# Kernel optimization log

Hardware: AMD Instinct MI355X
Metric: run time of the kernel (lower is better)

Reference implementation:

```python
import jax, jax.numpy as jnp
import numpy as np

N_EXPERTS = 8
TOP_K = 2
D_MODEL = 1024
HIDDEN = 4096


def setup_inputs() -> dict:
    key = jax.random.key(0)
    ks = jax.random.split(key, 6)
    B, S = 4, 1024
    scale = 0.02
    x = jax.random.normal(ks[0], (B, S, D_MODEL), dtype=jnp.float32)
    # gate / noise linear weights, torch nn.Linear convention: (out, in)
    w_gate = jax.random.normal(ks[1], (N_EXPERTS, D_MODEL), dtype=jnp.float32) * scale
    w_noise = jax.random.normal(ks[2], (N_EXPERTS, D_MODEL), dtype=jnp.float32) * scale
    # stacked expert weights: w_g/w_u: (E, H, D), w_d: (E, D, H)
    w_g = jax.random.normal(ks[3], (N_EXPERTS, HIDDEN, D_MODEL), dtype=jnp.float32) * scale
    w_u = jax.random.normal(ks[4], (N_EXPERTS, HIDDEN, D_MODEL), dtype=jnp.float32) * scale
    w_d = jax.random.normal(ks[5], (N_EXPERTS, D_MODEL, HIDDEN), dtype=jnp.float32) * scale
    return {"x": x, "w_gate": w_gate, "w_noise": w_noise, "w_g": w_g, "w_u": w_u, "w_d": w_d}


def reference(x, w_gate, w_noise, w_g, w_u, w_d):
    B, S, D = x.shape
    T = B * S
    xf = x.reshape(T, D)

    # --- NoisyTopKGate (eval mode: no noise) ---
    logits = xf @ w_gate.T                                  # (T, E)
    top_logits, top_idx = jax.lax.top_k(logits, TOP_K)      # (T, K)
    top_gates = jax.nn.softmax(top_logits, axis=-1)         # (T, K)
    rows = jnp.arange(T)[:, None]
    gates = jnp.zeros_like(logits).at[rows, top_idx].set(top_gates)  # (T, E) sparse

    probs = jax.nn.softmax(logits, axis=-1)
    f = gates.mean(axis=0)
    P = probs.mean(axis=0)
    aux_loss = N_EXPERTS * jnp.sum(f * P)

    # --- expert loop (SwiGLU FFN); gate==0 zeroes non-routed contributions ---
    out = jnp.zeros_like(xf)
    for e in range(N_EXPERTS):
        hidden = jax.nn.silu(xf @ w_g[e].T) * (xf @ w_u[e].T)   # (T, H)
        y = hidden @ w_d[e].T                                    # (T, D)
        out = out + gates[:, e:e + 1] * y

    return out.reshape(B, S, D), aux_loss
```

## Files before the change

### kernel.cpp

```cpp
#include <hip/hip_runtime.h>

#define TT 4096
#define DM 1024
#define HH 4096
#define NE 8
#define NSLOT (TT*2)
#define TM 128
#define MAXTILES 72

typedef __bf16 bf16x8 __attribute__((ext_vector_type(8)));
typedef float f32x4 __attribute__((ext_vector_type(4)));

__device__ __forceinline__ unsigned short f2bs(float f) {
  unsigned u = __float_as_uint(f);
  u += 0x7fffu + ((u >> 16) & 1u);
  return (unsigned short)(u >> 16);
}
__device__ __forceinline__ float bs2f(unsigned short s) {
  return __uint_as_float(((unsigned)s) << 16);
}
__device__ __forceinline__ unsigned pk_rnd(float lo, float hi) {
  return ((__float_as_uint(lo) + 0x8000u) >> 16) |
         ((__float_as_uint(hi) + 0x8000u) & 0xffff0000u);
}
__device__ __forceinline__ void gld_lds16(const unsigned short* g, unsigned short* l) {
  __builtin_amdgcn_global_load_lds(
      (const __attribute__((address_space(1))) unsigned int*)g,
      (__attribute__((address_space(3))) unsigned int*)l, 16, 0, 0);
}

__global__ __launch_bounds__(256) void k_gate(
    const float* __restrict__ x, const float* __restrict__ w_gate,
    int* __restrict__ counts, float* __restrict__ gsum, float* __restrict__ psum,
    int* __restrict__ gidx, float* __restrict__ gval) {
  __shared__ float wg[NE * DM];
  __shared__ float bg[NE]; __shared__ float bp[NE]; __shared__ int bc[NE];
  int tid = threadIdx.x;
  for (int i = tid; i < NE * DM; i += 256) wg[i] = w_gate[i];
  if (tid < NE) { bg[tid] = 0.f; bp[tid] = 0.f; bc[tid] = 0; }
  __syncthreads();
  int wave = tid >> 6, lane = tid & 63;
  for (int it = 0; it < 4; ++it) {
    int t = blockIdx.x * 16 + wave * 4 + it;
    const float* xr = x + (size_t)t * DM;
    float s[NE];
#pragma unroll
    for (int e = 0; e < NE; ++e) s[e] = 0.f;
    for (int d = lane; d < DM; d += 64) {
      float xv = xr[d];
#pragma unroll
      for (int e = 0; e < NE; ++e) s[e] += xv * wg[e * DM + d];
    }
#pragma unroll
    for (int e = 0; e < NE; ++e) {
      float v = s[e];
      v += __shfl_down(v, 32); v += __shfl_down(v, 16); v += __shfl_down(v, 8);
      v += __shfl_down(v, 4);  v += __shfl_down(v, 2);  v += __shfl_down(v, 1);
      s[e] = v;
    }
    if (lane == 0) {
      int e1 = 0; float v1 = s[0];
      for (int e = 1; e < NE; ++e) if (s[e] > v1) { v1 = s[e]; e1 = e; }
      int e2 = -1; float v2 = -1e30f;
      for (int e = 0; e < NE; ++e) if (e != e1 && s[e] > v2) { v2 = s[e]; e2 = e; }
      float g1 = 1.f / (1.f + __expf(v2 - v1));
      float g2 = 1.f - g1;
      float psm = 0.f, p[NE];
      for (int e = 0; e < NE; ++e) { p[e] = __expf(s[e] - v1); psm += p[e]; }
      float inv = 1.f / psm;
      atomicAdd(&bg[e1], g1); atomicAdd(&bg[e2], g2);
      for (int e = 0; e < NE; ++e) atomicAdd(&bp[e], p[e] * inv);
      atomicAdd(&bc[e1], 1); atomicAdd(&bc[e2], 1);
      gidx[t * 2] = e1; gidx[t * 2 + 1] = e2;
      gval[t * 2] = g1; gval[t * 2 + 1] = g2;
    }
  }
  __syncthreads();
  if (tid < NE) {
    atomicAdd(&counts[tid], bc[tid]);
    atomicAdd(&gsum[tid], bg[tid]);
    atomicAdd(&psum[tid], bp[tid]);
  }
}

__global__ void k_plan(const int* __restrict__ counts, const float* __restrict__ gsum,
                       const float* __restrict__ psum, int* __restrict__ bases,
                       int* __restrict__ ntiles, int* __restrict__ tile_e,
                       int* __restrict__ tile_s0, int* __restrict__ tile_n,
                       float* __restrict__ aux_out) {
  if (threadIdx.x != 0 || blockIdx.x != 0) return;
  int base = 0, nt = 0;
  for (int e = 0; e < NE; ++e) {
    bases[e] = base;
    int c = counts[e];
    for (int s = 0; s < c; s += TM) {
      tile_e[nt] = e; tile_s0[nt] = base + s;
      tile_n[nt] = (c - s < TM) ? (c - s) : TM; ++nt;
    }
    base += c;
  }
  *ntiles = nt;
  float aux = 0.f;
  for (int e = 0; e < NE; ++e)
    aux += (gsum[e] / (float)TT) * (psum[e] / (float)TT);
  *aux_out = aux * (float)NE;
}

__global__ __launch_bounds__(256) void k_scatter(
    const int* __restrict__ gidx, const int* __restrict__ bases,
    int* __restrict__ cursor, int* __restrict__ stok, int* __restrict__ t2s) {
  int t = blockIdx.x * 256 + threadIdx.x;
#pragma unroll
  for (int k = 0; k < 2; ++k) {
    int e = gidx[t * 2 + k];
    int pos = atomicAdd(&cursor[e], 1);
    int slot = bases[e] + pos;
    stok[slot] = t;
    t2s[t * 2 + k] = slot;
  }
}

__global__ __launch_bounds__(256) void k_gather(
    const float* __restrict__ x, const int* __restrict__ stok,
    unsigned short* __restrict__ abuf) {
  int gid = blockIdx.x * 256 + threadIdx.x;
  int slot = gid >> 7;
  int d0 = (gid & 127) << 3;
  int tok = stok[slot];
  const float* src = x + (size_t)tok * DM + d0;
  float4 v0 = *(const float4*)src;
  float4 v1 = *(const float4*)(src + 4);
  uint4 pk;
  pk.x = pk_rnd(v0.x, v0.y); pk.y = pk_rnd(v0.z, v0.w);
  pk.z = pk_rnd(v1.x, v1.y); pk.w = pk_rnd(v1.z, v1.w);
  *(uint4*)(abuf + (size_t)slot * DM + d0) = pk;
}


__global__ __launch_bounds__(256) void k_ffn1(
    const unsigned short* __restrict__ abuf, const float* __restrict__ w_g,
    const float* __restrict__ w_u, const int* __restrict__ ntiles,
    const int* __restrict__ tile_e, const int* __restrict__ tile_s0,
    const int* __restrict__ tile_n, unsigned short* __restrict__ hbuf) {
  int bid = blockIdx.x;
  int s = (bid & 7) * 576 + (bid >> 3);
  int mt = s % MAXTILES;
  int ny = s / MAXTILES;
  if (mt >= *ntiles) return;
  int e = tile_e[mt], s0 = tile_s0[mt], nrows = tile_n[mt];
  int n0 = ny * 64;
  __shared__ unsigned short As[TM * 64];
  __shared__ unsigned short Bg[64 * 64];
  __shared__ unsigned short Bu[64 * 64];
  int tid = threadIdx.x, wid = tid >> 6, lane = tid & 63;
  int wm = (wid >> 1) * 64, wn = (wid & 1) * 32;
  int l15 = lane & 15, lq = lane >> 4;
  int l8 = lane & 7, lr = lane >> 3;
  int scol = ((l8 ^ lr) << 3);

  const unsigned short* apA = abuf + (size_t)(s0 + wid * 32 + lr) * DM + scol;

  int br = tid >> 3, bb = tid & 7;
  int wb = ((bb ^ (br & 7)) << 3);
  const float* gp = w_g + ((size_t)e * HH + (size_t)(n0 + br)) * DM + bb * 8;
  const float* up = w_u + ((size_t)e * HH + (size_t)(n0 + br)) * DM + bb * 8;
  unsigned short* bg0 = Bg + br * 64 + wb;
  unsigned short* bu0 = Bu + br * 64 + wb;

  f32x4 accg[4][2], accu[4][2];
#pragma unroll
  for (int i = 0; i < 4; ++i)
#pragma unroll
    for (int j = 0; j < 2; ++j) {
      accg[i][j] = (f32x4){0.f, 0.f, 0.f, 0.f};
      accu[i][j] = (f32x4){0.f, 0.f, 0.f, 0.f};
    }

  for (int kb = 0; kb < DM; kb += 64) {
    __syncthreads();
#pragma unroll
    for (int c = 0; c < 4; ++c)
      gld_lds16(apA + kb + (size_t)c * 8 * DM, As + (wid * 32 + c * 8) * 64);
    float4 g0 = *(const float4*)(gp + kb);
    float4 g1 = *(const float4*)(gp + kb + 4);
    float4 g2 = *(const float4*)(gp + kb + (size_t)32 * DM);
    float4 g3 = *(const float4*)(gp + kb + (size_t)32 * DM + 4);
    float4 u0 = *(const float4*)(up + kb);
    float4 u1 = *(const float4*)(up + kb + 4);
    float4 u2 = *(const float4*)(up + kb + (size_t)32 * DM);
    float4 u3 = *(const float4*)(up + kb + (size_t)32 * DM + 4);
    uint4 p0, p1, q0, q1;
    p0.x = pk_rnd(g0.x, g0.y); p0.y = pk_rnd(g0.z, g0.w);
    p0.z = pk_rnd(g1.x, g1.y); p0.w = pk_rnd(g1.z, g1.w);
    p1.x = pk_rnd(g2.x, g2.y); p1.y = pk_rnd(g2.z, g2.w);
    p1.z = pk_rnd(g3.x, g3.y); p1.w = pk_rnd(g3.z, g3.w);
    q0.x = pk_rnd(u0.x, u0.y); q0.y = pk_rnd(u0.z, u0.w);
    q0.z = pk_rnd(u1.x, u1.y); q0.w = pk_rnd(u1.z, u1.w);
    q1.x = pk_rnd(u2.x, u2.y); q1.y = pk_rnd(u2.z, u2.w);
    q1.z = pk_rnd(u3.x, u3.y); q1.w = pk_rnd(u3.z, u3.w);
    *(uint4*)bg0 = p0;
    *(uint4*)(bg0 + 32 * 64) = p1;
    *(uint4*)bu0 = q0;
    *(uint4*)(bu0 + 32 * 64) = q1;
    __syncthreads();
    bf16x8 af[4][2], bgf[2][2], buf_[2][2];
#pragma unroll
    for (int mi = 0; mi < 4; ++mi) {
      int row = wm + mi * 16 + l15, sw = row & 7;
      af[mi][0] = *(const bf16x8*)&As[row * 64 + ((lq ^ sw) << 3)];
      af[mi][1] = *(const bf16x8*)&As[row * 64 + (((4 | lq) ^ sw) << 3)];
    }
#pragma unroll
    for (int ni = 0; ni < 2; ++ni) {
      int row = wn + ni * 16 + l15, sw = row & 7;
      bgf[ni][0] = *(const bf16x8*)&Bg[row * 64 + ((lq ^ sw) << 3)];
      bgf[ni][1] = *(const bf16x8*)&Bg[row * 64 + (((4 | lq) ^ sw) << 3)];
      buf_[ni][0] = *(const bf16x8*)&Bu[row * 64 + ((lq ^ sw) << 3)];
      buf_[ni][1] = *(const bf16x8*)&Bu[row * 64 + (((4 | lq) ^ sw) << 3)];
    }
#pragma unroll
    for (int kq = 0; kq < 2; ++kq)
#pragma unroll
      for (int mi = 0; mi < 4; ++mi)
#pragma unroll
        for (int ni = 0; ni < 2; ++ni) {
          accg[mi][ni] = __builtin_amdgcn_mfma_f32_16x16x32_bf16(
              af[mi][kq], bgf[ni][kq], accg[mi][ni], 0, 0, 0);
          accu[mi][ni] = __builtin_amdgcn_mfma_f32_16x16x32_bf16(
              af[mi][kq], buf_[ni][kq], accu[mi][ni], 0, 0, 0);
        }
  }

#pragma unroll
  for (int mi = 0; mi < 4; ++mi)
#pragma unroll
    for (int r = 0; r < 4; ++r) {
      int m_loc = wm + mi * 16 + lq * 4 + r;
      if (m_loc < nrows) {
#pragma unroll
        for (int ni = 0; ni < 2; ++ni) {
          float g = accg[mi][ni][r], u = accu[mi][ni][r];
          float h = g / (1.f + __expf(-g)) * u;
          int n = n0 + wn + ni * 16 + l15;
          hbuf[(size_t)(s0 + m_loc) * HH + n] = f2bs(h);
        }
      }
    }
}

__global__ __launch_bounds__(256) void k_ffn2(
    const unsigned short* __restrict__ hbuf, const float* __restrict__ w_d,
    const int* __restrict__ ntiles, const int* __restrict__ tile_e,
    const int* __restrict__ tile_s0, const int* __restrict__ tile_n,
    unsigned short* __restrict__ ybuf) {
  int bid = blockIdx.x;
  int s = (bid & 7) * 144 + (bid >> 3);
  int mt = s % MAXTILES;
  int ny = s / MAXTILES;
  if (mt >= *ntiles) return;
  int e = tile_e[mt], s0 = tile_s0[mt], nrows = tile_n[mt];
  int n0 = ny * 64;
  __shared__ unsigned short As[TM * 64];
  __shared__ unsigned short Bs[64 * 64];
  int tid = threadIdx.x, wid = tid >> 6, lane = tid & 63;
  int wm = (wid >> 1) * 64, wn = (wid & 1) * 32;
  int l15 = lane & 15, lq = lane >> 4;
  int l8 = lane & 7, lr = lane >> 3;
  int scol = ((l8 ^ lr) << 3);

  const unsigned short* apA = hbuf + (size_t)(s0 + wid * 32 + lr) * HH + scol;

  int br = tid >> 3, bb = tid & 7;
  int wb = ((bb ^ (br & 7)) << 3);
  const float* dp = w_d + ((size_t)e * DM + (size_t)(n0 + br)) * HH + bb * 8;
  unsigned short* bl0 = Bs + br * 64 + wb;

  f32x4 acc[4][2];
#pragma unroll
  for (int i = 0; i < 4; ++i)
#pragma unroll
    for (int j = 0; j < 2; ++j) acc[i][j] = (f32x4){0.f, 0.f, 0.f, 0.f};

  for (int kb = 0; kb < HH; kb += 64) {
    __syncthreads();
#pragma unroll
    for (int c = 0; c < 4; ++c)
      gld_lds16(apA + kb + (size_t)c * 8 * HH, As + (wid * 32 + c * 8) * 64);
    float4 d0 = *(const float4*)(dp + kb);
    float4 d1 = *(const float4*)(dp + kb + 4);
    float4 d2 = *(const float4*)(dp + kb + (size_t)32 * HH);
    float4 d3 = *(const float4*)(dp + kb + (size_t)32 * HH + 4);
    uint4 p0, p1;
    p0.x = pk_rnd(d0.x, d0.y); p0.y = pk_rnd(d0.z, d0.w);
    p0.z = pk_rnd(d1.x, d1.y); p0.w = pk_rnd(d1.z, d1.w);
    p1.x = pk_rnd(d2.x, d2.y); p1.y = pk_rnd(d2.z, d2.w);
    p1.z = pk_rnd(d3.x, d3.y); p1.w = pk_rnd(d3.z, d3.w);
    *(uint4*)bl0 = p0;
    *(uint4*)(bl0 + 32 * 64) = p1;
    __syncthreads();
    bf16x8 af[4][2], bf[2][2];
#pragma unroll
    for (int mi = 0; mi < 4; ++mi) {
      int row = wm + mi * 16 + l15, sw = row & 7;
      af[mi][0] = *(const bf16x8*)&As[row * 64 + ((lq ^ sw) << 3)];
      af[mi][1] = *(const bf16x8*)&As[row * 64 + (((4 | lq) ^ sw) << 3)];
    }
#pragma unroll
    for (int ni = 0; ni < 2; ++ni) {
      int row = wn + ni * 16 + l15, sw = row & 7;
      bf[ni][0] = *(const bf16x8*)&Bs[row * 64 + ((lq ^ sw) << 3)];
      bf[ni][1] = *(const bf16x8*)&Bs[row * 64 + (((4 | lq) ^ sw) << 3)];
    }
#pragma unroll
    for (int kq = 0; kq < 2; ++kq)
#pragma unroll
      for (int mi = 0; mi < 4; ++mi)
#pragma unroll
        for (int ni = 0; ni < 2; ++ni)
          acc[mi][ni] = __builtin_amdgcn_mfma_f32_16x16x32_bf16(
              af[mi][kq], bf[ni][kq], acc[mi][ni], 0, 0, 0);
  }

#pragma unroll
  for (int mi = 0; mi < 4; ++mi)
#pragma unroll
    for (int r = 0; r < 4; ++r) {
      int m_loc = wm + mi * 16 + lq * 4 + r;
      if (m_loc < nrows) {
#pragma unroll
        for (int ni = 0; ni < 2; ++ni) {
          int n = n0 + wn + ni * 16 + l15;
          ybuf[(size_t)(s0 + m_loc) * DM + n] = f2bs(acc[mi][ni][r]);
        }
      }
    }
}

__global__ __launch_bounds__(256) void k_combine(
    const unsigned short* __restrict__ ybuf, const int* __restrict__ t2s,
    const float* __restrict__ gval, float* __restrict__ out) {
  int gid = blockIdx.x * 256 + threadIdx.x;
  int t = gid >> 8;
  int d0 = (gid & 255) << 2;
  int s1 = t2s[t * 2], s2 = t2s[t * 2 + 1];
  float g1 = gval[t * 2], g2 = gval[t * 2 + 1];
  ushort4 y1 = *(const ushort4*)(ybuf + (size_t)s1 * DM + d0);
  ushort4 y2 = *(const ushort4*)(ybuf + (size_t)s2 * DM + d0);
  float4 o;
  o.x = g1 * bs2f(y1.x) + g2 * bs2f(y2.x);
  o.y = g1 * bs2f(y1.y) + g2 * bs2f(y2.y);
  o.z = g1 * bs2f(y1.z) + g2 * bs2f(y2.z);
  o.w = g1 * bs2f(y1.w) + g2 * bs2f(y2.w);
  *(float4*)(out + (size_t)t * DM + d0) = o;
}

extern "C" void kernel_launch(void* const* d_in, const int* in_sizes, int n_in,
                              void* d_out, int out_size, void* d_ws, size_t ws_size,
                              hipStream_t stream) {
  const float* x      = (const float*)d_in[0];
  const float* w_gate = (const float*)d_in[1];
  const float* w_g    = (const float*)d_in[3];
  const float* w_u    = (const float*)d_in[4];
  const float* w_d    = (const float*)d_in[5];
  float* out = (float*)d_out;

  char* ws = (char*)d_ws;
  int*   counts  = (int*)(ws + 0);
  int*   cursor  = (int*)(ws + 32);
  float* gsum    = (float*)(ws + 64);
  float* psum    = (float*)(ws + 96);
  int*   ntiles  = (int*)(ws + 128);
  int*   bases   = (int*)(ws + 192);
  int*   tile_e  = (int*)(ws + 4096);
  int*   tile_s0 = (int*)(ws + 4608);
  int*   tile_n  = (int*)(ws + 5120);
  int*   gidx    = (int*)(ws + 16384);
  float* gval    = (float*)(ws + 49152);
  int*   stok    = (int*)(ws + 81920);
  int*   t2s     = (int*)(ws + 114688);
  unsigned short* abuf = (unsigned short*)(ws + (1ull << 20));
  unsigned short* ybuf = abuf;
  unsigned short* hbuf = (unsigned short*)(ws + (18ull << 20));

  hipMemsetAsync(ws, 0, 256, stream);
  k_gate<<<256, 256, 0, stream>>>(x, w_gate, counts, gsum, psum, gidx, gval);
  k_plan<<<1, 64, 0, stream>>>(counts, gsum, psum, bases, ntiles, tile_e, tile_s0,
                               tile_n, out + (size_t)TT * DM);
  k_scatter<<<TT / 256, 256, 0, stream>>>(gidx, bases, cursor, stok, t2s);
  k_gather<<<NSLOT * 128 / 256, 256, 0, stream>>>(x, stok, abuf);
  k_ffn1<<<MAXTILES * (HH / 64), 256, 0, stream>>>(abuf, w_g, w_u, ntiles,
                                                   tile_e, tile_s0, tile_n, hbuf);
  k_ffn2<<<MAXTILES * (DM / 64), 256, 0, stream>>>(hbuf, w_d, ntiles, tile_e,
                                                   tile_s0, tile_n, ybuf);
  k_combine<<<(TT * DM / 4) / 256, 256, 0, stream>>>(ybuf, t2s, gval, out);
}
```

Baseline: 801.8 us.

## Double-buffer LDS tiles in expert FFN GEMMs to overlap loads with MFMA

Both expert GEMM kernels now keep two LDS buffers for the A and B tiles. The global loads and LDS DMA for the next K-step are issued before the MFMAs on the current buffer, and the converted weights are written to LDS afterward, which cuts the loop to one barrier per iteration and hides global latency behind compute. The fp32-to-bf16 packing also switches from manual bit rounding to a native bf16 conversion. The cost is doubled LDS use, which may lower occupancy, and the prefetched float4 values held across the MFMAs raise register pressure.

```diff
diff --git a/kernel.cpp b/kernel.cpp
--- a/kernel.cpp
+++ b/kernel.cpp
@@ -9,6 +9,7 @@
 #define MAXTILES 72
 
 typedef __bf16 bf16x8 __attribute__((ext_vector_type(8)));
+typedef __bf16 bf16x2_t __attribute__((ext_vector_type(2)));
 typedef float f32x4 __attribute__((ext_vector_type(4)));
 
 __device__ __forceinline__ unsigned short f2bs(float f) {
@@ -18,6 +19,10 @@
 }
 __device__ __forceinline__ float bs2f(unsigned short s) {
   return __uint_as_float(((unsigned)s) << 16);
+}
+__device__ __forceinline__ unsigned pk2(float lo, float hi) {
+  bf16x2_t v; v[0] = (__bf16)lo; v[1] = (__bf16)hi;
+  union { bf16x2_t b; unsigned u; } c; c.b = v; return c.u;
 }
 __device__ __forceinline__ unsigned pk_rnd(float lo, float hi) {
   return ((__float_as_uint(lo) + 0x8000u) >> 16) |
@@ -149,9 +154,9 @@
   if (mt >= *ntiles) return;
   int e = tile_e[mt], s0 = tile_s0[mt], nrows = tile_n[mt];
   int n0 = ny * 64;
-  __shared__ unsigned short As[TM * 64];
-  __shared__ unsigned short Bg[64 * 64];
-  __shared__ unsigned short Bu[64 * 64];
+  __shared__ unsigned short As[2][TM * 64];
+  __shared__ unsigned short Bg[2][64 * 64];
+  __shared__ unsigned short Bu[2][64 * 64];
   int tid = threadIdx.x, wid = tid >> 6, lane = tid & 63;
   int wm = (wid >> 1) * 64, wn = (wid & 1) * 32;
   int l15 = lane & 15, lq = lane >> 4;
@@ -164,8 +169,44 @@
   int wb = ((bb ^ (br & 7)) << 3);
   const float* gp = w_g + ((size_t)e * HH + (size_t)(n0 + br)) * DM + bb * 8;
   const float* up = w_u + ((size_t)e * HH + (size_t)(n0 + br)) * DM + bb * 8;
-  unsigned short* bg0 = Bg + br * 64 + wb;
-  unsigned short* bu0 = Bu + br * 64 + wb;
+
+  float4 g0, g1, g2, g3, u0, u1, u2, u3;
+
+#define FFN1_LOADB(KB)                                                      \
+  do {                                                                      \
+    g0 = *(const float4*)(gp + (KB));                                       \
+    g1 = *(const float4*)(gp + (KB) + 4);                                   \
+    g2 = *(const float4*)(gp + (KB) + (size_t)32 * DM);                     \
+    g3 = *(const float4*)(gp + (KB) + (size_t)32 * DM + 4);                 \
+    u0 = *(const float4*)(up + (KB));                                       \
+    u1 = *(const float4*)(up + (KB) + 4);                                   \
+    u2 = *(const float4*)(up + (KB) + (size_t)32 * DM);                     \
+    u3 = *(const float4*)(up + (KB) + (size_t)32 * DM + 4);                 \
+  } while (0)
+
+#define FFN1_GLDA(KB, P)                                                    \
+  do {                                                                      \
+    _Pragma("unroll") for (int c = 0; c < 4; ++c)                           \
+        gld_lds16(apA + (KB) + (size_t)c * 8 * DM,                          \
+                  As[P] + (wid * 32 + c * 8) * 64);                         \
+  } while (0)
+
+#define FFN1_WRITEB(P)                                                      \
+  do {                                                                      \
+    uint4 p0, p1, q0, q1;                                                   \
+    p0.x = pk2(g0.x, g0.y); p0.y = pk2(g0.z, g0.w);                         \
+    p0.z = pk2(g1.x, g1.y); p0.w = pk2(g1.z, g1.w);                         \
+    p1.x = pk2(g2.x, g2.y); p1.y = pk2(g2.z, g2.w);                         \
+    p1.z = pk2(g3.x, g3.y); p1.w = pk2(g3.z, g3.w);                         \
+    q0.x = pk2(u0.x, u0.y); q0.y = pk2(u0.z, u0.w);                         \
+    q0.z = pk2(u1.x, u1.y); q0.w = pk2(u1.z, u1.w);                         \
+    q1.x = pk2(u2.x, u2.y); q1.y = pk2(u2.z, u2.w);                         \
+    q1.z = pk2(u3.x, u3.y); q1.w = pk2(u3.z, u3.w);                         \
+    *(uint4*)(Bg[P] + br * 64 + wb) = p0;                                   \
+    *(uint4*)(Bg[P] + (br + 32) * 64 + wb) = p1;                            \
+    *(uint4*)(Bu[P] + br * 64 + wb) = q0;                                   \
+    *(uint4*)(Bu[P] + (br + 32) * 64 + wb) = q1;                            \
+  } while (0)
 
   f32x4 accg[4][2], accu[4][2];
 #pragma unroll
@@ -176,47 +217,30 @@
       accu[i][j] = (f32x4){0.f, 0.f, 0.f, 0.f};
     }
 
+  FFN1_LOADB(0);
+  FFN1_GLDA(0, 0);
+  FFN1_WRITEB(0);
+  __syncthreads();
+
+  int p = 0;
   for (int kb = 0; kb < DM; kb += 64) {
-    __syncthreads();
-#pragma unroll
-    for (int c = 0; c < 4; ++c)
-      gld_lds16(apA + kb + (size_t)c * 8 * DM, As + (wid * 32 + c * 8) * 64);
-    float4 g0 = *(const float4*)(gp + kb);
-    float4 g1 = *(const float4*)(gp + kb + 4);
-    float4 g2 = *(const float4*)(gp + kb + (size_t)32 * DM);
-    float4 g3 = *(const float4*)(gp + kb + (size_t)32 * DM + 4);
-    float4 u0 = *(const float4*)(up + kb);
-    float4 u1 = *(const float4*)(up + kb + 4);
-    float4 u2 = *(const float4*)(up + kb + (size_t)32 * DM);
-    float4 u3 = *(const float4*)(up + kb + (size_t)32 * DM + 4);
-    uint4 p0, p1, q0, q1;
-    p0.x = pk_rnd(g0.x, g0.y); p0.y = pk_rnd(g0.z, g0.w);
-    p0.z = pk_rnd(g1.x, g1.y); p0.w = pk_rnd(g1.z, g1.w);
-    p1.x = pk_rnd(g2.x, g2.y); p1.y = pk_rnd(g2.z, g2.w);
-    p1.z = pk_rnd(g3.x, g3.y); p1.w = pk_rnd(g3.z, g3.w);
-    q0.x = pk_rnd(u0.x, u0.y); q0.y = pk_rnd(u0.z, u0.w);
-    q0.z = pk_rnd(u1.x, u1.y); q0.w = pk_rnd(u1.z, u1.w);
-    q1.x = pk_rnd(u2.x, u2.y); q1.y = pk_rnd(u2.z, u2.w);
-    q1.z = pk_rnd(u3.x, u3.y); q1.w = pk_rnd(u3.z, u3.w);
-    *(uint4*)bg0 = p0;
-    *(uint4*)(bg0 + 32 * 64) = p1;
-    *(uint4*)bu0 = q0;
-    *(uint4*)(bu0 + 32 * 64) = q1;
-    __syncthreads();
+    int q = p ^ 1;
+    bool more = (kb + 64 < DM);
+    if (more) { FFN1_LOADB(kb + 64); FFN1_GLDA(kb + 64, q); }
     bf16x8 af[4][2], bgf[2][2], buf_[2][2];
 #pragma unroll
     for (int mi = 0; mi < 4; ++mi) {
       int row = wm + mi * 16 + l15, sw = row & 7;
-      af[mi][0] = *(const bf16x8*)&As[row * 64 + ((lq ^ sw) << 3)];
-      af[mi][1] = *(const bf16x8*)&As[row * 64 + (((4 | lq) ^ sw) << 3)];
+      af[mi][0] = *(const bf16x8*)&As[p][row * 64 + ((lq ^ sw) << 3)];
+      af[mi][1] = *(const bf16x8*)&As[p][row * 64 + (((4 | lq) ^ sw) << 3)];
     }
 #pragma unroll
     for (int ni = 0; ni < 2; ++ni) {
       int row = wn + ni * 16 + l15, sw = row & 7;
-      bgf[ni][0] = *(const bf16x8*)&Bg[row * 64 + ((lq ^ sw) << 3)];
-      bgf[ni][1] = *(const bf16x8*)&Bg[row * 64 + (((4 | lq) ^ sw) << 3)];
-      buf_[ni][0] = *(const bf16x8*)&Bu[row * 64 + ((lq ^ sw) << 3)];
-      buf_[ni][1] = *(const bf16x8*)&Bu[row * 64 + (((4 | lq) ^ sw) << 3)];
+      bgf[ni][0] = *(const bf16x8*)&Bg[p][row * 64 + ((lq ^ sw) << 3)];
+      bgf[ni][1] = *(const bf16x8*)&Bg[p][row * 64 + (((4 | lq) ^ sw) << 3)];
+      buf_[ni][0] = *(const bf16x8*)&Bu[p][row * 64 + ((lq ^ sw) << 3)];
+      buf_[ni][1] = *(const bf16x8*)&Bu[p][row * 64 + (((4 | lq) ^ sw) << 3)];
     }
 #pragma unroll
     for (int kq = 0; kq < 2; ++kq)
@@ -229,6 +253,9 @@
           accu[mi][ni] = __builtin_amdgcn_mfma_f32_16x16x32_bf16(
               af[mi][kq], buf_[ni][kq], accu[mi][ni], 0, 0, 0);
         }
+    if (more) FFN1_WRITEB(q);
+    __syncthreads();
+    p = q;
   }
 
 #pragma unroll
@@ -260,8 +287,8 @@
   if (mt >= *ntiles) return;
   int e = tile_e[mt], s0 = tile_s0[mt], nrows = tile_n[mt];
   int n0 = ny * 64;
-  __shared__ unsigned short As[TM * 64];
-  __shared__ unsigned short Bs[64 * 64];
+  __shared__ unsigned short As[2][TM * 64];
+  __shared__ unsigned short Bs[2][64 * 64];
   int tid = threadIdx.x, wid = tid >> 6, lane = tid & 63;
   int wm = (wid >> 1) * 64, wn = (wid & 1) * 32;
   int l15 = lane & 15, lq = lane >> 4;
@@ -273,7 +300,34 @@
   int br = tid >> 3, bb = tid & 7;
   int wb = ((bb ^ (br & 7)) << 3);
   const float* dp = w_d + ((size_t)e * DM + (size_t)(n0 + br)) * HH + bb * 8;
-  unsigned short* bl0 = Bs + br * 64 + wb;
+
+  float4 d0, d1, d2, d3;
+
+#define FFN2_LOADB(KB)                                                      \
+  do {                                                                      \
+    d0 = *(const float4*)(dp + (KB));                                       \
+    d1 = *(const float4*)(dp + (KB) + 4);                                   \
+    d2 = *(const float4*)(dp + (KB) + (size_t)32 * HH);                     \
+    d3 = *(const float4*)(dp + (KB) + (size_t)32 * HH + 4);                 \
+  } while (0)
+
+#define FFN2_GLDA(KB, P)                                                    \
+  do {                                                                      \
+    _Pragma("unroll") for (int c = 0; c < 4; ++c)                           \
+        gld_lds16(apA + (KB) + (size_t)c * 8 * HH,                          \
+                  As[P] + (wid * 32 + c * 8) * 64);                         \
+  } while (0)
+
+#define FFN2_WRITEB(P)                                                      \
+  do {                                                                      \
+    uint4 p0, p1;                                                           \
+    p0.x = pk2(d0.x, d0.y); p0.y = pk2(d0.z, d0.w);                         \
+    p0.z = pk2(d1.x, d1.y); p0.w = pk2(d1.z, d1.w);                         \
+    p1.x = pk2(d2.x, d2.y); p1.y = pk2(d2.z, d2.w);                         \
+    p1.z = pk2(d3.x, d3.y); p1.w = pk2(d3.z, d3.w);                         \
+    *(uint4*)(Bs[P] + br * 64 + wb) = p0;                                   \
+    *(uint4*)(Bs[P] + (br + 32) * 64 + wb) = p1;                            \
+  } while (0)
 
   f32x4 acc[4][2];
 #pragma unroll
@@ -281,35 +335,28 @@
 #pragma unroll
     for (int j = 0; j < 2; ++j) acc[i][j] = (f32x4){0.f, 0.f, 0.f, 0.f};
 
+  FFN2_LOADB(0);
+  FFN2_GLDA(0, 0);
+  FFN2_WRITEB(0);
+  __syncthreads();
+
+  int p = 0;
   for (int kb = 0; kb < HH; kb += 64) {
-    __syncthreads();
-#pragma unroll
-    for (int c = 0; c < 4; ++c)
-      gld_lds16(apA + kb + (size_t)c * 8 * HH, As + (wid * 32 + c * 8) * 64);
-    float4 d0 = *(const float4*)(dp + kb);
-    float4 d1 = *(const float4*)(dp + kb + 4);
-    float4 d2 = *(const float4*)(dp + kb + (size_t)32 * HH);
-    float4 d3 = *(const float4*)(dp + kb + (size_t)32 * HH + 4);
-    uint4 p0, p1;
-    p0.x = pk_rnd(d0.x, d0.y); p0.y = pk_rnd(d0.z, d0.w);
-    p0.z = pk_rnd(d1.x, d1.y); p0.w = pk_rnd(d1.z, d1.w);
-    p1.x = pk_rnd(d2.x, d2.y); p1.y = pk_rnd(d2.z, d2.w);
-    p1.z = pk_rnd(d3.x, d3.y); p1.w = pk_rnd(d3.z, d3.w);
-    *(uint4*)bl0 = p0;
-    *(uint4*)(bl0 + 32 * 64) = p1;
-    __syncthreads();
+    int q = p ^ 1;
+    bool more = (kb + 64 < HH);
+    if (more) { FFN2_LOADB(kb + 64); FFN2_GLDA(kb + 64, q); }
     bf16x8 af[4][2], bf[2][2];
 #pragma unroll
     for (int mi = 0; mi < 4; ++mi) {
       int row = wm + mi * 16 + l15, sw = row & 7;
-      af[mi][0] = *(const bf16x8*)&As[row * 64 + ((lq ^ sw) << 3)];
-      af[mi][1] = *(const bf16x8*)&As[row * 64 + (((4 | lq) ^ sw) << 3)];
+      af[mi][0] = *(const bf16x8*)&As[p][row * 64 + ((lq ^ sw) << 3)];
+      af[mi][1] = *(const bf16x8*)&As[p][row * 64 + (((4 | lq) ^ sw) << 3)];
     }
 #pragma unroll
     for (int ni = 0; ni < 2; ++ni) {
       int row = wn + ni * 16 + l15, sw = row & 7;
-      bf[ni][0] = *(const bf16x8*)&Bs[row * 64 + ((lq ^ sw) << 3)];
-      bf[ni][1] = *(const bf16x8*)&Bs[row * 64 + (((4 | lq) ^ sw) << 3)];
+      bf[ni][0] = *(const bf16x8*)&Bs[p][row * 64 + ((lq ^ sw) << 3)];
+      bf[ni][1] = *(const bf16x8*)&Bs[p][row * 64 + (((4 | lq) ^ sw) << 3)];
     }
 #pragma unroll
     for (int kq = 0; kq < 2; ++kq)
@@ -319,6 +366,9 @@
         for (int ni = 0; ni < 2; ++ni)
           acc[mi][ni] = __builtin_amdgcn_mfma_f32_16x16x32_bf16(
               af[mi][kq], bf[ni][kq], acc[mi][ni], 0, 0, 0);
+    if (more) FFN2_WRITEB(q);
+    __syncthreads();
+    p = q;
   }
 
 #pragma unroll
```

Result: slower. 829.6 us (+3.5%).
